# Kernel optimization log

Hardware: AMD Instinct MI355X
Metric: run time of the kernel (lower is better)

Reference implementation:

```python
import jax, jax.numpy as jnp
import numpy as np

T = 1_000_000          # number of t_eval points (~1 year at 30 s)
N_ROOMS = 10
N = 12                 # 2 latent wall nodes + n_rooms
DT = 30.0              # seconds between t_eval points
LOAD_SCALE = 50.0      # physical_cooling_scaling: W/m^2 scale for sigmoid(loads)


def setup_inputs() -> dict:
    key = jax.random.key(0)
    k1, k2, k3, k4, k5 = jax.random.split(key, 5)
    t_eval = jnp.arange(T, dtype=jnp.float32) * DT
    x0 = 26.0 * jnp.ones((N,), jnp.float32)  # reset_iv: 26 C at every node
    # Stable slow RC dynamics: negative-definite-ish A with small coupling
    A = (-1e-5 * jnp.eye(N, dtype=jnp.float32)
         + 1e-6 * jax.random.normal(k1, (N, N), jnp.float32))
    B = 1e-6 * jax.random.normal(k2, (N, 1 + N_ROOMS), jnp.float32)
    Tout_data = 10.0 + 20.0 * jax.random.uniform(k3, (T,), jnp.float32)  # outdoor temp samples on t_eval grid
    loads_raw = jax.random.normal(k4, (2, N_ROOMS), jnp.float32)         # pre-sigmoid [cool; gain] loads
    room_areas = 10.0 + 40.0 * jax.random.uniform(k5, (N_ROOMS,), jnp.float32)
    return {"t_eval": t_eval, "x0": x0, "A": A, "B": B,
            "Tout_data": Tout_data, "loads_raw": loads_raw, "room_areas": room_areas}


def reference(t_eval, x0, A, B, Tout_data, loads_raw, room_areas):
    # transform + physical scaling of loads (self.transform = sigmoid)
    loads = jax.nn.sigmoid(loads_raw) * LOAD_SCALE
    cool_load, gain_load = loads[0], loads[1]
    action = 0.0  # no cooling policy -> self.action stays 0
    Q_area = -cool_load * action + gain_load            # [n_rooms]
    Q_watts = Q_area * room_areas                        # proportional_heating
    # u = [Tout; Q_watts] so B@u = B[:,0]*Tout + B[:,1:]@Q_watts (Q constant over t)
    b0 = B[:, 0]                                         # [N]
    Bq = B[:, 1:] @ Q_watts                              # [N], constant forcing
    h = t_eval[1] - t_eval[0]                            # uniform step
    # Linear interp of Tout: value at t_i, midpoint t_i+h/2, and t_{i+1}
    To_t = Tout_data[:-1]
    To_n = Tout_data[1:]
    To_m = 0.5 * (To_t + To_n)

    def f(x, To):  # dy/dt = A x + B u
        return A @ x + b0 * To + Bq

    def step(x, tou):
        to_t, to_m, to_n = tou
        k1 = f(x, to_t)
        k2 = f(x + 0.5 * h * k1, to_m)
        k3 = f(x + 0.5 * h * k2, to_m)
        k4 = f(x + h * k3, to_n)
        xn = x + (h / 6.0) * (k1 + 2.0 * k2 + 2.0 * k3 + k4)
        return xn, xn

    _, xs = jax.lax.scan(step, x0, (To_t, To_m, To_n))
    return jnp.concatenate([x0[None, :], xs], axis=0)  # [T, N]
```

## Files before the change

### kernel.cpp

```cpp
#include <hip/hip_runtime.h>
#include <math.h>


#define S_STEPS 999999
#define CH      8
#define BLK     256
#define NB_W    489
#define NCHUNK  125000
#define LASTFULL 124998

#define OFF_M   0
#define OFF_C   144
#define OFF_AL  156
#define OFF_BE  168
#define OFF_K   192
#define OFF_P2  320
#define OFF_PA  1472
#define OFF_PL  1616
#define OFF_PD  2048
#define NCONS   3200
#define NS1Q    368
#define NS2Q    432
#define OFF_AGG 3200
#define OFF_FLAG 9072
#define OFF_SFLAG 9568
#define MAGIC1  0x1357ACE9
#define MAGIC2  0x2468BDF1

#define FMA4(Q,a,b,c,d,acc) fmaf((Q).w,(d),fmaf((Q).z,(c),fmaf((Q).y,(b),fmaf((Q).x,(a),(acc)))))

__device__ __forceinline__ void mv_acc(const float* Pf, const float* x, float* y) {
  const float4* P = reinterpret_cast<const float4*>(Pf);
#pragma unroll
  for (int i = 0; i < 12; ++i) {
    float4 a = P[3*i], b = P[3*i+1], c = P[3*i+2];
    y[i] = FMA4(c, x[8],x[9],x[10],x[11],
            FMA4(b, x[4],x[5],x[6],x[7],
             FMA4(a, x[0],x[1],x[2],x[3], y[i])));
  }
}

__device__ __forceinline__ float rowdot(const float* Prow, const float* xv) {
  const float4* P = reinterpret_cast<const float4*>(Prow);
  float4 a = P[0], b = P[1], c = P[2];
  return FMA4(c, xv[8],xv[9],xv[10],xv[11],
          FMA4(b, xv[4],xv[5],xv[6],xv[7],
           FMA4(a, xv[0],xv[1],xv[2],xv[3], 0.f)));
}

__device__ __forceinline__ void fold_chunk(const float* cons,
                                           const float* tos, float* v) {
  const float4* Kq = reinterpret_cast<const float4*>(cons + OFF_K);
  float4 c0=Kq[0], c1=Kq[1], c2=Kq[2];
  v[0]=c0.x; v[1]=c0.y; v[2]=c0.z; v[3]=c0.w;
  v[4]=c1.x; v[5]=c1.y; v[6]=c1.z; v[7]=c1.w;
  v[8]=c2.x; v[9]=c2.y; v[10]=c2.z; v[11]=c2.w;
#pragma unroll
  for (int s = 0; s < 9; ++s) {
    float ts = tos[s];
    float4 ka=Kq[3*(s+1)], kb=Kq[3*(s+1)+1], kc=Kq[3*(s+1)+2];
    v[0]=fmaf(ka.x,ts,v[0]); v[1]=fmaf(ka.y,ts,v[1]); v[2]=fmaf(ka.z,ts,v[2]); v[3]=fmaf(ka.w,ts,v[3]);
    v[4]=fmaf(kb.x,ts,v[4]); v[5]=fmaf(kb.y,ts,v[5]); v[6]=fmaf(kb.z,ts,v[6]); v[7]=fmaf(kb.w,ts,v[7]);
    v[8]=fmaf(kc.x,ts,v[8]); v[9]=fmaf(kc.y,ts,v[9]); v[10]=fmaf(kc.z,ts,v[10]); v[11]=fmaf(kc.w,ts,v[11]);
  }
}

__global__ void __launch_bounds__(BLK, 2) fused_all(
    const float* __restrict__ t_eval, const float* __restrict__ A,
    const float* __restrict__ Bm, const float* __restrict__ loads_raw,
    const float* __restrict__ areas,
    float* ws, const float* __restrict__ To,
    const float* __restrict__ x0, float* __restrict__ out) {
  __shared__ __align__(16) float Lc[NCONS];
  __shared__ __align__(16) float Tw[48];
  __shared__ __align__(16) float Ta[24];
  __shared__ __align__(16) float Pw[48];
  __shared__ __align__(16) float lkb[32*12];
  __shared__ __align__(16) float yv[8*12];
  __shared__ __align__(16) float zv[8*12];
  __shared__ __align__(16) float Xs[12];
  __shared__ __align__(16) float Qw[48];
  __shared__ double H1[144], H2[144], H3[144], H4[144], Md[144];
  __shared__ double Qa[144], Qb[144];
  __shared__ double C512s[144], C1024s[144], C2048s[144], C4096s[144];
  __shared__ double C8192s[144], C16384s[144], C32768s[144], Pd3s[144];
  __shared__ double cd[12], ald[12], bed[12], b0d[12], bqd[12];
  __shared__ double Vv[3][12], Kd[120];

  int k = threadIdx.x;
  float* agg   = ws + OFF_AGG;
  int*   flags = (int*)(ws + OFF_FLAG);
  int*   sflag = (int*)(ws + OFF_SFLAG);

  if (blockIdx.x == 0) {
    int t = k;
    for (int f = t; f < NB_W; f += BLK) flags[f] = 0;
    double h = (double)t_eval[1] - (double)t_eval[0];
    if (t < 144) H1[t] = h * (double)A[t];
    if (t < 12) {
      b0d[t] = (double)Bm[t*11];
      double s = 0.0;
      for (int r = 0; r < 10; ++r) {
        double gq = 50.0 / (1.0 + exp(-(double)loads_raw[10 + r]));
        s += (double)Bm[t*11 + 1 + r] * (gq * (double)areas[r]);
      }
      bqd[t] = s;
    }
    if (t < 120) Kd[t] = 0.0;
    __syncthreads();
    if (t < 144) {
      int i=t/12, j=t%12; double s=0.0;
#pragma unroll
      for (int m = 0; m < 12; ++m) s += H1[i*12+m]*H1[m*12+j];
      H2[t]=s;
    }
    __syncthreads();
    for (int e2 = t; e2 < 288; e2 += BLK) {
      int w=e2/144, e=e2%144, i=e/12, j=e%12;
      const double* Bp = w ? H2 : H1;
      double s = 0.0;
#pragma unroll
      for (int m = 0; m < 12; ++m) s += H2[i*12+m]*Bp[m*12+j];
      (w ? H4 : H3)[e] = s;
    }
    __syncthreads();
    if (t < 12) {
      double hb=0,h2b=0,h3b=0,hb0=0,h2b0=0,h3b0=0;
#pragma unroll
      for (int m = 0; m < 12; ++m) {
        hb  += H1[t*12+m]*bqd[m]; h2b  += H2[t*12+m]*bqd[m]; h3b  += H3[t*12+m]*bqd[m];
        hb0 += H1[t*12+m]*b0d[m]; h2b0 += H2[t*12+m]*b0d[m]; h3b0 += H3[t*12+m]*b0d[m];
      }
      double h6 = h / 6.0;
      cd[t]  = h6*(6.0*bqd[t] + 3.0*hb + h2b + 0.25*h3b);
      ald[t] = h6*(3.0*b0d[t] + 2.0*hb0 + 0.75*h2b0 + 0.25*h3b0);
      bed[t] = h6*(3.0*b0d[t] + hb0 + 0.25*h2b0);
      Vv[0][t]=ald[t]; Vv[1][t]=bed[t]; Vv[2][t]=cd[t];
      Kd[96+t] += ald[t]; Kd[108+t] += bed[t]; Kd[t] += cd[t];
    }
    if (t < 144) {
      int i=t/12, j=t%12;
      Md[t] = (i==j ? 1.0 : 0.0) + H1[t] + 0.5*H2[t] + H3[t]/6.0 + H4[t]/24.0;
    }
    __syncthreads();
    if (t < 144) { ws[OFF_M+t] = (float)Md[t]; Qa[t] = Md[t]; }
    if (t < 12) {
      ws[OFF_C+t]=(float)cd[t]; ws[OFF_AL+t]=(float)ald[t]; ws[OFF_BE+t]=(float)bed[t];
    }
    __syncthreads();
    double* src = Qa; double* dst = Qb;
    for (int r = 1; r <= 15; ++r) {
      double acc = 0.0, ks = 0.0;
      if (t < 144) {
        int i=t/12, j=t%12;
#pragma unroll
        for (int m = 0; m < 12; ++m) acc += src[i*12+m]*src[m*12+j];
      }
      int w=0, i2=0;
      if (r <= 7 && t >= 144 && t < 180) {
        w=(t-144)/12; i2=(t-144)%12;
#pragma unroll
        for (int m = 0; m < 12; ++m) ks += Md[i2*12+m]*Vv[w][m];
      }
      __syncthreads();
      if (t < 144) {
        dst[t] = acc;
        if (r >= 3 && r <= 8) ws[OFF_P2+(r-3)*144+t] = (float)acc;
        if (r == 9)  { ws[OFF_P2+6*144+t] = (float)acc; C512s[t]=acc; }
        if (r == 10) { ws[OFF_P2+7*144+t] = (float)acc; C1024s[t]=acc; }
        if (r == 11) { ws[OFF_PL+t]       = (float)acc; C2048s[t]=acc; }
        if (r == 12) { ws[OFF_PL+144+t]   = (float)acc; C4096s[t]=acc; }
        if (r == 13) { ws[OFF_PD+144+t]   = (float)acc; C8192s[t]=acc; }
        if (r == 14) { ws[OFF_PD+2*144+t] = (float)acc; C16384s[t]=acc; }
        if (r == 15) { ws[OFF_PD+4*144+t] = (float)acc; C32768s[t]=acc; }
        if (r == 8)  ws[OFF_PD+t] = (t % 13 == 0) ? 1.f : 0.f;
      }
      if (r <= 7 && t >= 144 && t < 180) {
        Vv[w][i2] = ks;
        if (w == 0) Kd[(8-r)*12+i2] += ks;
        else if (w == 1) Kd[(9-r)*12+i2] += ks;
        else Kd[i2] += ks;
      }
      if (r == 8 && t < 120) ws[OFF_K+t] = (float)Kd[t];
      __syncthreads();
      double* tmp = src; src = dst; dst = tmp;
      if (r == 10 && t == 0)
        __hip_atomic_store(&sflag[0], MAGIC1, __ATOMIC_RELEASE,
                           __HIP_MEMORY_SCOPE_AGENT);
    }
    for (int idx = t; idx < 432; idx += BLK) {
      int w=idx/144, e=idx%144, i=e/12, j=e%12;
      const double* Ap = (w==0) ? C512s  : ((w==1) ? C2048s : C8192s);
      const double* Bp = (w==0) ? C1024s : ((w==1) ? C4096s : C16384s);
      double s = 0.0;
#pragma unroll
      for (int m = 0; m < 12; ++m) s += Ap[i*12+m]*Bp[m*12+j];
      if (w==0) ws[OFF_PA+e] = (float)s;
      else if (w==1) ws[OFF_PL+2*144+e] = (float)s;
      else { ws[OFF_PD+3*144+e] = (float)s; Pd3s[e] = s; }
    }
    __syncthreads();
    for (int idx = t; idx < 432; idx += BLK) {
      int w=idx/144, e=idx%144, i=e/12, j=e%12;
      const double* Ap = (w==0) ? C8192s : ((w==1) ? C16384s : Pd3s);
      double s = 0.0;
#pragma unroll
      for (int m = 0; m < 12; ++m) s += Ap[i*12+m]*C32768s[m*12+j];
      ws[OFF_PD+(5+w)*144+e] = (float)s;
    }
    __syncthreads();
    if (t == 0)
      __hip_atomic_store(&sflag[1], MAGIC2, __ATOMIC_RELEASE,
                         __HIP_MEMORY_SCOPE_AGENT);
    return;
  }

  int b = blockIdx.x - 1;
  int g = b*BLK + k, base = g*CH;
  bool active = (g < NCHUNK), fullc = (g <= LASTFULL);
  float to_[9];
#pragma unroll
  for (int i = 0; i < 9; ++i) to_[i] = 0.f;
  if (active) {
    const float4* tp = reinterpret_cast<const float4*>(To + base);
    float4 ta = tp[0], tb = tp[1];
    to_[0]=ta.x; to_[1]=ta.y; to_[2]=ta.z; to_[3]=ta.w;
    to_[4]=tb.x; to_[5]=tb.y; to_[6]=tb.z; to_[7]=tb.w;
    to_[8] = fullc ? To[base+8] : 0.f;
  }
  if (k == 0) {
    while (__hip_atomic_load(&sflag[0], __ATOMIC_RELAXED,
                             __HIP_MEMORY_SCOPE_AGENT) != MAGIC1)
      __builtin_amdgcn_s_sleep(8);
    (void)__hip_atomic_load(&sflag[0], __ATOMIC_ACQUIRE,
                            __HIP_MEMORY_SCOPE_AGENT);
  }
  __syncthreads();
  {
    const float4* s4 = reinterpret_cast<const float4*>(ws);
    float4* d4 = reinterpret_cast<float4*>(Lc);
#pragma unroll
    for (int r = 0; r < 2; ++r) {
      int idx = k + r*BLK;
      if (idx < NS1Q) d4[idx] = s4[idx];
    }
  }
  __syncthreads();
  const float* lc = Lc;
  float v[12];
  if (fullc) fold_chunk(lc, to_, v);
  else {
#pragma unroll
    for (int i = 0; i < 12; ++i) v[i] = 0.f;
  }
  if (g == 0) {
    float xi[12];
#pragma unroll
    for (int i = 0; i < 12; ++i) xi[i] = x0[i];
    mv_acc(lc + OFF_P2, xi, v);
  }
  int j = k & 63, w = k >> 6;
#pragma unroll
  for (int l = 0; l < 6; ++l) {
    int off = 1 << l;
    float nb[12];
#pragma unroll
    for (int i = 0; i < 12; ++i) nb[i] = __shfl_up(v[i], (unsigned)off, 64);
    if (j >= off) mv_acc(lc + OFF_P2 + l*144, nb, v);
  }
  float se[12];
#pragma unroll
  for (int i = 0; i < 12; ++i) {
    float u = __shfl_up(v[i], 1u, 64);
    se[i] = (j == 0) ? 0.f : u;
  }
  if (j == 63) {
#pragma unroll
    for (int i = 0; i < 12; ++i) Tw[w*12 + i] = v[i];
  }
  __syncthreads();
  if (k < 24) {
    int p = k/12, comp = k - p*12;
    Ta[k] = rowdot(lc + OFF_P2 + 6*144 + comp*12, Tw + 2*p*12)
          + Tw[(2*p+1)*12 + comp];
  }
  __syncthreads();
  if (k < 12) {
    float val = rowdot(lc + OFF_P2 + 7*144 + k*12, Ta) + Ta[12 + k];
    __hip_atomic_store(&agg[b*12 + k], val, __ATOMIC_RELAXED,
                       __HIP_MEMORY_SCOPE_AGENT);
  }
  __syncthreads();
  if (k == 0)
    __hip_atomic_store(&flags[b], 1, __ATOMIC_RELEASE,
                       __HIP_MEMORY_SCOPE_AGENT);
  if (k < 32) {
    int src = b - 1 - k;
    if (src >= 0) {
      while (__hip_atomic_load(&flags[src], __ATOMIC_ACQUIRE,
                               __HIP_MEMORY_SCOPE_AGENT) == 0) {
        __builtin_amdgcn_s_sleep(1);
      }
    }
  } else if (k == 32) {
    while (__hip_atomic_load(&sflag[1], __ATOMIC_RELAXED,
                             __HIP_MEMORY_SCOPE_AGENT) != MAGIC2)
      __builtin_amdgcn_s_sleep(2);
    (void)__hip_atomic_load(&sflag[1], __ATOMIC_ACQUIRE,
                            __HIP_MEMORY_SCOPE_AGENT);
  }
  __syncthreads();
  {
    const float4* s4 = reinterpret_cast<const float4*>(ws);
    float4* d4 = reinterpret_cast<float4*>(Lc);
#pragma unroll
    for (int r = 0; r < 2; ++r) {
      int idx = k + r*BLK;
      if (idx < NS2Q) d4[NS1Q + idx] = s4[NS1Q + idx];
    }
  }
  __syncthreads();
#pragma unroll
  for (int r = 0; r < 2; ++r) {
    int idx = k + r*BLK;
    if (idx < 384) {
      int slot = idx / 12, comp = idx - slot*12;
      int src = b - 1 - slot;
      float acc = 0.f;
      if (src >= 0) {
        int jj = slot & 3;
        const float* ag = agg + src*12;
        acc = (jj == 0) ? ag[comp]
            : rowdot(lc + OFF_PL + (jj-1)*144 + comp*12, ag);
      }
      lkb[idx] = acc;
    }
  }
  __syncthreads();
  if (k < 96) {
    int i = k/12, comp = k - i*12;
    yv[k] = lkb[(4*i)*12+comp] + lkb[(4*i+1)*12+comp]
          + lkb[(4*i+2)*12+comp] + lkb[(4*i+3)*12+comp];
  } else if (k >= 192 && k < 216) {
    int q = k - 192;
    if (q < 12) Pw[q] = 0.f;
    else Pw[q] = Tw[q-12];
  }
  __syncthreads();
  if (k < 96) {
    int i = k/12, comp = k - i*12;
    zv[k] = (i == 0) ? yv[comp]
          : rowdot(lc + OFF_PD + i*144 + comp*12, yv + i*12);
  } else if (k >= 192 && k < 204) {
    int comp = k - 192;
    Pw[24+comp] = rowdot(lc + OFF_P2 + 6*144 + comp*12, Pw+12) + Tw[12+comp];
  }
  __syncthreads();
  if (k < 12) {
    float s = 0.f;
#pragma unroll
    for (int i = 0; i < 8; ++i) s += zv[i*12 + k];
    Xs[k] = s;
  } else if (k >= 192 && k < 204) {
    int comp = k - 192;
    Pw[36+comp] = rowdot(lc + OFF_P2 + 6*144 + comp*12, Pw+24) + Tw[24+comp];
  }
  __syncthreads();
  if (k < 48) {
    int ww = k/12, comp = k - ww*12;
    float acc;
    if (ww == 0) acc = Xs[comp];
    else if (ww == 1) acc = rowdot(lc + OFF_P2 + 6*144 + comp*12, Xs);
    else if (ww == 2) acc = rowdot(lc + OFF_P2 + 7*144 + comp*12, Xs);
    else acc = rowdot(lc + OFF_PA + comp*12, Xs);
    Qw[k] = acc + Pw[k];
  }
  __syncthreads();
  if (!active) return;
  float x[12];
#pragma unroll
  for (int i = 0; i < 12; ++i) x[i] = Qw[w*12 + i];
#pragma unroll
  for (int l = 0; l < 6; ++l) {
    if ((j >> l) & 1) {
      float vn[12];
#pragma unroll
      for (int i = 0; i < 12; ++i) vn[i] = 0.f;
      mv_acc(lc + OFF_P2 + l*144, x, vn);
#pragma unroll
      for (int i = 0; i < 12; ++i) x[i] = vn[i];
    }
  }
#pragma unroll
  for (int i = 0; i < 12; ++i) x[i] += se[i];
  if (b == 0 && k == 0) {
#pragma unroll
    for (int i = 0; i < 12; ++i) x[i] += x0[i];
#pragma unroll
    for (int i = 0; i < 12; ++i) out[i] = x0[i];
  }
  float cv[12], av[12], bv[12];
#pragma unroll
  for (int i = 0; i < 12; ++i) {
    cv[i] = lc[OFF_C + i]; av[i] = lc[OFF_AL + i]; bv[i] = lc[OFF_BE + i];
  }
  const float4* Mq = reinterpret_cast<const float4*>(lc + OFF_M);
#pragma unroll
  for (int s = 0; s < CH; ++s) {
    float tot = to_[s], ton = to_[s+1];
    float xn[12];
#pragma unroll
    for (int i = 0; i < 12; ++i) {
      float4 a = Mq[3*i], bq = Mq[3*i+1], c = Mq[3*i+2];
      xn[i] = FMA4(c, x[8],x[9],x[10],x[11],
               FMA4(bq, x[4],x[5],x[6],x[7],
                FMA4(a, x[0],x[1],x[2],x[3],
                 fmaf(bv[i],ton,fmaf(av[i],tot,cv[i])))));
    }
    int tt = base + s;
    if (tt < S_STEPS) {
      float4* op = reinterpret_cast<float4*>(out + (size_t)(tt+1)*12);
      op[0] = make_float4(xn[0],xn[1],xn[2],xn[3]);
      op[1] = make_float4(xn[4],xn[5],xn[6],xn[7]);
      op[2] = make_float4(xn[8],xn[9],xn[10],xn[11]);
    }
#pragma unroll
    for (int i = 0; i < 12; ++i) x[i] = xn[i];
  }
}

extern "C" void kernel_launch(void* const* d_in, const int* in_sizes, int n_in,
                              void* d_out, int out_size, void* d_ws, size_t ws_size,
                              hipStream_t stream) {
  const float* t_eval    = (const float*)d_in[0];
  const float* x0        = (const float*)d_in[1];
  const float* A         = (const float*)d_in[2];
  const float* B         = (const float*)d_in[3];
  const float* To        = (const float*)d_in[4];
  const float* loads_raw = (const float*)d_in[5];
  const float* areas     = (const float*)d_in[6];
  float* out = (float*)d_out;
  float* ws  = (float*)d_ws;

  fused_all<<<NB_W + 1, BLK, 0, stream>>>(t_eval, A, B, loads_raw, areas,
                                          ws, To, x0, out);
}
```

Before: 133.2 us.

## Split setup-block handshake into three flags and read late constants from global

The setup block now publishes its constants in three stages. Worker blocks can start the chunk fold and the first five scan levels once the step matrices are ready, then wait for the level-5 matrix and stage it into LDS. The lookback and decoupling matrices are read straight from the global workspace instead of being copied to shared memory, which shrinks the LDS footprint. The final stepping loop also hoists the 12x12 step matrix into registers, at the cost of higher register pressure under launch bounds of 2 blocks.

```diff
diff --git a/kernel.cpp b/kernel.cpp
--- a/kernel.cpp
+++ b/kernel.cpp
@@ -18,14 +18,15 @@
 #define OFF_PA  1472
 #define OFF_PL  1616
 #define OFF_PD  2048
-#define NCONS   3200
-#define NS1Q    368
-#define NS2Q    432
+#define NLC     1472
+#define NS1AQ   260
+#define NS1BQ   108
 #define OFF_AGG 3200
 #define OFF_FLAG 9072
 #define OFF_SFLAG 9568
-#define MAGIC1  0x1357ACE9
-#define MAGIC2  0x2468BDF1
+#define MAGICA  0x1357ACE9
+#define MAGICB  0x2468BDF1
+#define MAGICC  0x369CF258
 
 #define FMA4(Q,a,b,c,d,acc) fmaf((Q).w,(d),fmaf((Q).z,(c),fmaf((Q).y,(b),fmaf((Q).x,(a),(acc)))))
 
@@ -71,7 +72,7 @@
     const float* __restrict__ areas,
     float* ws, const float* __restrict__ To,
     const float* __restrict__ x0, float* __restrict__ out) {
-  __shared__ __align__(16) float Lc[NCONS];
+  __shared__ __align__(16) float Lc[NLC];
   __shared__ __align__(16) float Tw[48];
   __shared__ __align__(16) float Ta[24];
   __shared__ __align__(16) float Pw[48];
@@ -181,11 +182,17 @@
         else if (w == 1) Kd[(9-r)*12+i2] += ks;
         else Kd[i2] += ks;
       }
-      if (r == 8 && t < 120) ws[OFF_K+t] = (float)Kd[t];
       __syncthreads();
       double* tmp = src; src = dst; dst = tmp;
+      if (r == 7) {
+        if (t < 120) ws[OFF_K+t] = (float)Kd[t];
+        __syncthreads();
+        if (t == 0)
+          __hip_atomic_store(&sflag[0], MAGICA, __ATOMIC_RELEASE,
+                             __HIP_MEMORY_SCOPE_AGENT);
+      }
       if (r == 10 && t == 0)
-        __hip_atomic_store(&sflag[0], MAGIC1, __ATOMIC_RELEASE,
+        __hip_atomic_store(&sflag[1], MAGICB, __ATOMIC_RELEASE,
                            __HIP_MEMORY_SCOPE_AGENT);
     }
     for (int idx = t; idx < 432; idx += BLK) {
@@ -210,7 +217,7 @@
     }
     __syncthreads();
     if (t == 0)
-      __hip_atomic_store(&sflag[1], MAGIC2, __ATOMIC_RELEASE,
+      __hip_atomic_store(&sflag[2], MAGICC, __ATOMIC_RELEASE,
                          __HIP_MEMORY_SCOPE_AGENT);
     return;
   }
@@ -230,7 +237,7 @@
   }
   if (k == 0) {
     while (__hip_atomic_load(&sflag[0], __ATOMIC_RELAXED,
-                             __HIP_MEMORY_SCOPE_AGENT) != MAGIC1)
+                             __HIP_MEMORY_SCOPE_AGENT) != MAGICA)
       __builtin_amdgcn_s_sleep(8);
     (void)__hip_atomic_load(&sflag[0], __ATOMIC_ACQUIRE,
                             __HIP_MEMORY_SCOPE_AGENT);
@@ -242,7 +249,7 @@
 #pragma unroll
     for (int r = 0; r < 2; ++r) {
       int idx = k + r*BLK;
-      if (idx < NS1Q) d4[idx] = s4[idx];
+      if (idx < NS1AQ) d4[idx] = s4[idx];
     }
   }
   __syncthreads();
@@ -261,12 +268,32 @@
   }
   int j = k & 63, w = k >> 6;
 #pragma unroll
-  for (int l = 0; l < 6; ++l) {
+  for (int l = 0; l < 5; ++l) {
     int off = 1 << l;
     float nb[12];
 #pragma unroll
     for (int i = 0; i < 12; ++i) nb[i] = __shfl_up(v[i], (unsigned)off, 64);
     if (j >= off) mv_acc(lc + OFF_P2 + l*144, nb, v);
+  }
+  if (k == 0) {
+    while (__hip_atomic_load(&sflag[1], __ATOMIC_RELAXED,
+                             __HIP_MEMORY_SCOPE_AGENT) != MAGICB)
+      __builtin_amdgcn_s_sleep(2);
+    (void)__hip_atomic_load(&sflag[1], __ATOMIC_ACQUIRE,
+                            __HIP_MEMORY_SCOPE_AGENT);
+  }
+  __syncthreads();
+  {
+    const float4* s4 = reinterpret_cast<const float4*>(ws);
+    float4* d4 = reinterpret_cast<float4*>(Lc);
+    if (k < NS1BQ) d4[NS1AQ + k] = s4[NS1AQ + k];
+  }
+  __syncthreads();
+  {
+    float nb[12];
+#pragma unroll
+    for (int i = 0; i < 12; ++i) nb[i] = __shfl_up(v[i], 32u, 64);
+    if (j >= 32) mv_acc(lc + OFF_P2 + 5*144, nb, v);
   }
   float se[12];
 #pragma unroll
@@ -303,21 +330,11 @@
       }
     }
   } else if (k == 32) {
-    while (__hip_atomic_load(&sflag[1], __ATOMIC_RELAXED,
-                             __HIP_MEMORY_SCOPE_AGENT) != MAGIC2)
+    while (__hip_atomic_load(&sflag[2], __ATOMIC_RELAXED,
+                             __HIP_MEMORY_SCOPE_AGENT) != MAGICC)
       __builtin_amdgcn_s_sleep(2);
-    (void)__hip_atomic_load(&sflag[1], __ATOMIC_ACQUIRE,
+    (void)__hip_atomic_load(&sflag[2], __ATOMIC_ACQUIRE,
                             __HIP_MEMORY_SCOPE_AGENT);
-  }
-  __syncthreads();
-  {
-    const float4* s4 = reinterpret_cast<const float4*>(ws);
-    float4* d4 = reinterpret_cast<float4*>(Lc);
-#pragma unroll
-    for (int r = 0; r < 2; ++r) {
-      int idx = k + r*BLK;
-      if (idx < NS2Q) d4[NS1Q + idx] = s4[NS1Q + idx];
-    }
   }
   __syncthreads();
 #pragma unroll
@@ -331,7 +348,7 @@
         int jj = slot & 3;
         const float* ag = agg + src*12;
         acc = (jj == 0) ? ag[comp]
-            : rowdot(lc + OFF_PL + (jj-1)*144 + comp*12, ag);
+            : rowdot(ws + OFF_PL + (jj-1)*144 + comp*12, ag);
       }
       lkb[idx] = acc;
     }
@@ -350,7 +367,7 @@
   if (k < 96) {
     int i = k/12, comp = k - i*12;
     zv[k] = (i == 0) ? yv[comp]
-          : rowdot(lc + OFF_PD + i*144 + comp*12, yv + i*12);
+          : rowdot(ws + OFF_PD + i*144 + comp*12, yv + i*12);
   } else if (k >= 192 && k < 204) {
     int comp = k - 192;
     Pw[24+comp] = rowdot(lc + OFF_P2 + 6*144 + comp*12, Pw+12) + Tw[12+comp];
@@ -372,7 +389,7 @@
     if (ww == 0) acc = Xs[comp];
     else if (ww == 1) acc = rowdot(lc + OFF_P2 + 6*144 + comp*12, Xs);
     else if (ww == 2) acc = rowdot(lc + OFF_P2 + 7*144 + comp*12, Xs);
-    else acc = rowdot(lc + OFF_PA + comp*12, Xs);
+    else acc = rowdot(ws + OFF_PA + comp*12, Xs);
     Qw[k] = acc + Pw[k];
   }
   __syncthreads();
@@ -405,18 +422,27 @@
     cv[i] = lc[OFF_C + i]; av[i] = lc[OFF_AL + i]; bv[i] = lc[OFF_BE + i];
   }
   const float4* Mq = reinterpret_cast<const float4*>(lc + OFF_M);
+  float4 m0 =Mq[0],  m1 =Mq[1],  m2 =Mq[2],  m3 =Mq[3],  m4 =Mq[4],  m5 =Mq[5];
+  float4 m6 =Mq[6],  m7 =Mq[7],  m8 =Mq[8],  m9 =Mq[9],  m10=Mq[10], m11=Mq[11];
+  float4 m12=Mq[12], m13=Mq[13], m14=Mq[14], m15=Mq[15], m16=Mq[16], m17=Mq[17];
+  float4 m18=Mq[18], m19=Mq[19], m20=Mq[20], m21=Mq[21], m22=Mq[22], m23=Mq[23];
+  float4 m24=Mq[24], m25=Mq[25], m26=Mq[26], m27=Mq[27], m28=Mq[28], m29=Mq[29];
+  float4 m30=Mq[30], m31=Mq[31], m32=Mq[32], m33=Mq[33], m34=Mq[34], m35=Mq[35];
+#define EROW(i, A, B, Cq) \
+  xn[i] = FMA4(Cq, x[8],x[9],x[10],x[11], \
+           FMA4(B, x[4],x[5],x[6],x[7], \
+            FMA4(A, x[0],x[1],x[2],x[3], \
+             fmaf(bv[i],ton,fmaf(av[i],tot,cv[i])))))
 #pragma unroll
   for (int s = 0; s < CH; ++s) {
     float tot = to_[s], ton = to_[s+1];
     float xn[12];
-#pragma unroll
-    for (int i = 0; i < 12; ++i) {
-      float4 a = Mq[3*i], bq = Mq[3*i+1], c = Mq[3*i+2];
-      xn[i] = FMA4(c, x[8],x[9],x[10],x[11],
-               FMA4(bq, x[4],x[5],x[6],x[7],
-                FMA4(a, x[0],x[1],x[2],x[3],
-                 fmaf(bv[i],ton,fmaf(av[i],tot,cv[i])))));
-    }
+    EROW(0,  m0,  m1,  m2);  EROW(1,  m3,  m4,  m5);
+    EROW(2,  m6,  m7,  m8);  EROW(3,  m9,  m10, m11);
+    EROW(4,  m12, m13, m14); EROW(5,  m15, m16, m17);
+    EROW(6,  m18, m19, m20); EROW(7,  m21, m22, m23);
+    EROW(8,  m24, m25, m26); EROW(9,  m27, m28, m29);
+    EROW(10, m30, m31, m32); EROW(11, m33, m34, m35);
     int tt = base + s;
     if (tt < S_STEPS) {
       float4* op = reinterpret_cast<float4*>(out + (size_t)(tt+1)*12);
@@ -427,6 +453,7 @@
 #pragma unroll
     for (int i = 0; i < 12; ++i) x[i] = xn[i];
   }
+#undef EROW
 }
 
 extern "C" void kernel_launch(void* const* d_in, const int* in_sizes, int n_in,
```

Measured after the change: 132.2 us. Within noise of the previous version (-0.8%).
